# Performance work log

Measured on AMD Instinct MI355X. Metric: run time of the kernel, lower is better.

Reference implementation:

```python
import jax, jax.numpy as jnp
import numpy as np

EMBED_DIM = 256
NUM_HEADS = 4
HEAD_DIM = EMBED_DIM // NUM_HEADS
B, N0, N1 = 4, 2048, 2048


def setup_inputs() -> dict:
    key = jax.random.key(0)
    ks = jax.random.split(key, 16)
    d = EMBED_DIM
    s = 0.02
    return {
        "x0": jax.random.normal(ks[0], (B, N0, d), jnp.float32),
        "x1": jax.random.normal(ks[1], (B, N1, d), jnp.float32),
        "Wqk": jax.random.normal(ks[2], (d, d), jnp.float32) * s,
        "bqk": jnp.zeros((d,), jnp.float32),
        "Wv": jax.random.normal(ks[3], (d, d), jnp.float32) * s,
        "bv": jnp.zeros((d,), jnp.float32),
        "Wout": jax.random.normal(ks[4], (d, d), jnp.float32) * s,
        "bout": jnp.zeros((d,), jnp.float32),
        "W0": jax.random.normal(ks[5], (2 * d, 2 * d), jnp.float32) * s,
        "b0": jnp.zeros((2 * d,), jnp.float32),
        "ln_scale": jnp.ones((2 * d,), jnp.float32),
        "ln_bias": jnp.zeros((2 * d,), jnp.float32),
        "W3": jax.random.normal(ks[6], (2 * d, d), jnp.float32) * s,
        "b3": jnp.zeros((d,), jnp.float32),
    }


def _heads(t, b, n):
    # [b, n, d] -> [b, h, n, hd]
    return t.reshape(b, n, NUM_HEADS, HEAD_DIM).transpose(0, 2, 1, 3)


def _layernorm(y, scale, bias, eps=1e-5):
    mu = jnp.mean(y, axis=-1, keepdims=True)
    var = jnp.mean(jnp.square(y - mu), axis=-1, keepdims=True)
    return (y - mu) * jax.lax.rsqrt(var + eps) * scale + bias


def reference(x0, x1, Wqk, bqk, Wv, bv, Wout, bout, W0, b0, ln_scale, ln_bias, W3, b3):
    b, n0, d = x0.shape
    _, n1, _ = x1.shape
    scale = 1.0 / jnp.sqrt(jnp.float32(HEAD_DIM))

    qk0 = _heads(x0 @ Wqk + bqk, b, n0)
    qk1 = _heads(x1 @ Wqk + bqk, b, n1)
    v0 = _heads(x0 @ Wv + bv, b, n0)
    v1 = _heads(x1 @ Wv + bv, b, n1)

    # shared logits: [b, h, n0, n1]
    logits01 = jnp.einsum('bhid,bhjd->bhij', qk0, qk1) * scale
    attn01 = jax.nn.softmax(logits01, axis=-1)
    m0 = jnp.einsum('bhij,bhjd->bhid', attn01, v1)
    attn10 = jax.nn.softmax(logits01.transpose(0, 1, 3, 2), axis=-1)
    m1 = jnp.einsum('bhji,bhjd->bhid', attn10.transpose(0, 1, 3, 2), v0)

    m0 = m0.transpose(0, 2, 1, 3).reshape(b, n0, d) @ Wout + bout
    m1 = m1.transpose(0, 2, 1, 3).reshape(b, n1, d) @ Wout + bout

    def ffn(x, m):
        y = jnp.concatenate([x, m], axis=-1) @ W0 + b0
        y = _layernorm(y, ln_scale, ln_bias)
        y = jax.nn.gelu(y, approximate=False)
        return x + y @ W3 + b3

    return ffn(x0, m0), ffn(x1, m1)
```

## Files before the change

kernel.cpp:

```cpp
#include <hip/hip_runtime.h>
#include <math.h>

#define BATCH 4
#define SEQ 2048
#define DMODEL 256
#define NH 4
#define HD 64
#define MROWS 8192
#define QKSCALE 0.4246608905f

typedef short bf16x8 __attribute__((ext_vector_type(8)));
typedef float f32x4 __attribute__((ext_vector_type(4)));
typedef unsigned short us;

#if __has_builtin(__builtin_amdgcn_exp2f)
#define EXP2(x) __builtin_amdgcn_exp2f(x)
#else
#define EXP2(x) exp2f(x)
#endif

__device__ __forceinline__ us f2bf(float x) {
  union { float f; unsigned int u; } v;
  v.f = x;
  unsigned int r = (v.u + 0x7FFF + ((v.u >> 16) & 1)) >> 16;
  return (us)r;
}
__device__ __forceinline__ float bf2f(us u) {
  union { unsigned int u; float f; } v;
  v.u = ((unsigned int)u) << 16;
  return v.f;
}
__device__ __forceinline__ unsigned int fbits(float x) {
  union { float f; unsigned int u; } v;
  v.f = x;
  return v.u;
}
__device__ __forceinline__ unsigned int pk2bf(float lo, float hi) {
  return __builtin_amdgcn_perm(fbits(hi), fbits(lo), 0x07060302u);
}
__device__ __forceinline__ void dma16(const void* g, void* l) {
  auto gp = (const __attribute__((address_space(1))) unsigned int*)(unsigned long long)(uintptr_t)g;
  auto lp = (__attribute__((address_space(3))) unsigned int*)(unsigned int)(uintptr_t)l;
  __builtin_amdgcn_global_load_lds(gp, lp, 16, 0, 0);
}

__global__ __launch_bounds__(256) void cast_x(
    const float* __restrict__ x0, const float* __restrict__ x1,
    us* __restrict__ x0b, us* __restrict__ x1b) {
  const int n4 = (MROWS * DMODEL) / 4;
  int i = blockIdx.x * 256 + threadIdx.x;
  const float* src = (i < n4) ? x0 : x1;
  us* dst = (i < n4) ? x0b : x1b;
  int j = (i < n4) ? i : i - n4;
  float4 v = *(const float4*)&src[j * 4];
  ushort4 o = {f2bf(v.x), f2bf(v.y), f2bf(v.z), f2bf(v.w)};
  *(ushort4*)&dst[j * 4] = o;
}

__global__ __launch_bounds__(256) void cast_w(
    const float* __restrict__ Wqk, const float* __restrict__ Wv,
    const float* __restrict__ W0, const float* __restrict__ W3,
    const float* __restrict__ bqk, const float* __restrict__ bv,
    us* __restrict__ Wqvt, us* __restrict__ W1t, us* __restrict__ W3t,
    float* __restrict__ bias_qv) {
  int gid = blockIdx.x * 256 + threadIdx.x;
  if (gid < 65536) {
    int k = gid >> 8, j = gid & 255;
    Wqvt[j * 256 + k] = f2bf(Wqk[gid]);
  } else if (gid < 131072) {
    int i = gid - 65536;
    int k = i >> 8, j = i & 255;
    Wqvt[(256 + j) * 256 + k] = f2bf(Wv[i]);
  } else if (gid < 262144) {
    int i = gid - 131072;
    int k = i >> 9, j = i & 511;
    W1t[j * 512 + k] = f2bf(W0[i]);
  } else if (gid < 393216) {
    int i = gid - 262144;
    int k = i >> 8, j = i & 255;
    W3t[j * 512 + k] = f2bf(W3[i]);
  } else if (gid < 393728) {
    int j = gid - 393216;
    bias_qv[j] = (j < 256) ? bqk[j] : bv[j - 256];
  }
}

__global__ __launch_bounds__(256) void wcomb_k(
    const float* __restrict__ Wout, const float* __restrict__ W0,
    const float* __restrict__ b0, const float* __restrict__ bout,
    us* __restrict__ W1t, float* __restrict__ bias1) {
  int t = threadIdx.x, i = blockIdx.x;
  if (i < 256) {
    float a0 = 0.f, a1 = 0.f;
    for (int k0 = 0; k0 < 256; k0 += 8) {
      float wk[8], r0[8], r1[8];
#pragma unroll
      for (int u = 0; u < 8; ++u) {
        wk[u] = Wout[i * 256 + k0 + u];
        const float* row = &W0[(size_t)(256 + k0 + u) * 512];
        r0[u] = row[t];
        r1[u] = row[t + 256];
      }
#pragma unroll
      for (int u = 0; u < 8; ++u) { a0 += wk[u] * r0[u]; a1 += wk[u] * r1[u]; }
    }
    W1t[t * 512 + 256 + i] = f2bf(a0);
    W1t[(t + 256) * 512 + 256 + i] = f2bf(a1);
  } else {
    float a0 = b0[t], a1 = b0[t + 256];
    for (int k = 0; k < 256; ++k) {
      float bk = bout[k];
      const float* row = &W0[(size_t)(256 + k) * 512];
      a0 += bk * row[t];
      a1 += bk * row[t + 256];
    }
    bias1[t] = a0;
    bias1[t + 256] = a1;
  }
}

template <int MODE>
__global__ __launch_bounds__(256) void gemm4(
    const us* __restrict__ A0, const us* __restrict__ A1,
    const us* __restrict__ Am0, const us* __restrict__ Am1,
    const us* __restrict__ Wt, const float* __restrict__ bias,
    const float* __restrict__ r0_, const float* __restrict__ r1_,
    void* __restrict__ C0_, void* __restrict__ C1_,
    void* __restrict__ V0_, void* __restrict__ V1_, int K) {
  __shared__ us lds[17408];

  const int t = threadIdx.x, w = t >> 6, lane = t & 63;
  const int qd = lane >> 4, l15 = lane & 15;
  const int qr = w >> 1, qc = w & 1;
  const int row0 = blockIdx.x * 128;
  const int coltile = blockIdx.y, col0 = coltile * 128;
  const int z = blockIdx.z;
  const us* Ax = z ? A1 : A0;
  const us* Am = z ? Am1 : Am0;

  f32x4 acc[4][4];
#pragma unroll
  for (int i = 0; i < 4; ++i)
#pragma unroll
    for (int j = 0; j < 4; ++j) acc[i][j] = (f32x4){0.f, 0.f, 0.f, 0.f};

  for (int k0 = 0; k0 < K; k0 += 64) {
    __syncthreads();
#pragma unroll
    for (int pp = 0; pp < 8; ++pp) {
      int g = pp * 4 + w;
      const us* src;
      if (g < 16) {
        int tm = g >> 1, s = g & 1;
        const us* Ap = Ax;
        int kk = k0 + s * 32 + qd * 8;
        int lda = K;
        if (MODE == 1) {
          Ap = (k0 < 256) ? Ax : Am;
          kk = kk & 255;
          lda = 256;
        }
        src = &Ap[(size_t)(row0 + tm * 16 + l15) * lda + kk];
      } else {
        int gb = g - 16, tn = gb >> 1, s = gb & 1;
        src = &Wt[(size_t)(col0 + tn * 16 + l15) * K + k0 + s * 32 + qd * 8];
      }
      dma16(src, &lds[g * 512]);
    }
    __syncthreads();

#pragma unroll
    for (int s = 0; s < 2; ++s) {
      bf16x8 af[4], bfr[4];
#pragma unroll
      for (int i = 0; i < 4; ++i) {
        af[i] = *(const bf16x8*)&lds[(((qr * 4 + i) * 2 + s) * 64 + lane) * 8];
        bfr[i] = *(const bf16x8*)&lds[8192 + (((qc * 4 + i) * 2 + s) * 64 + lane) * 8];
      }
#pragma unroll
      for (int i = 0; i < 4; ++i)
#pragma unroll
        for (int j = 0; j < 4; ++j)
          acc[i][j] = __builtin_amdgcn_mfma_f32_16x16x32_bf16(af[i], bfr[j], acc[i][j], 0, 0, 0);
    }
  }

  if (MODE == 0 && coltile >= 2) {
    __syncthreads();
    int base = qc * 8320;
#pragma unroll
    for (int j = 0; j < 4; ++j) {
      int col = col0 + qc * 64 + j * 16 + l15;
      float bb = bias[col];
#pragma unroll
      for (int i = 0; i < 4; ++i)
#pragma unroll
        for (int r = 0; r < 4; ++r)
          lds[base + (j * 16 + l15) * 130 + (qr * 64 + i * 16 + qd * 4 + r)] =
              f2bf(acc[i][j][r] + bb);
    }
    __syncthreads();
    us* Vt = (us*)(z ? V1_ : V0_);
    int b_ = row0 >> 11, seq0 = row0 & 2047;
    for (int c = t; c < 2048; c += 256) {
      int hh = c >> 10, cc = c & 1023;
      int dloc = cc >> 4, scc = cc & 15;
      int h = (coltile - 2) * 2 + hh;
      uint4 d = *(const uint4*)&lds[hh * 8320 + dloc * 130 + scc * 8];
      *(uint4*)&Vt[((size_t)(b_ * NH + h) * HD + dloc) * SEQ + seq0 + scc * 8] = d;
    }
    return;
  }

#pragma unroll
  for (int j = 0; j < 4; ++j) {
    int col = col0 + qc * 64 + j * 16 + l15;
    float bb = bias[col];
#pragma unroll
    for (int i = 0; i < 4; ++i)
#pragma unroll
      for (int r = 0; r < 4; ++r) {
        size_t grow = row0 + qr * 64 + i * 16 + qd * 4 + r;
        float v = acc[i][j][r] + bb;
        if (MODE == 0) {
          ((us*)(z ? C1_ : C0_))[grow * 256 + col] = f2bf(v * QKSCALE);
        } else if (MODE == 1) {
          ((us*)(z ? C1_ : C0_))[grow * 512 + col] = f2bf(v);
        } else {
          const float* R = z ? r1_ : r0_;
          ((float*)(z ? C1_ : C0_))[grow * 256 + col] = R[grow * 256 + col] + v;
        }
      }
  }
}

__global__ __launch_bounds__(256) void flash_v6(
    const us* __restrict__ qk0, const us* __restrict__ qk1,
    const us* __restrict__ vt0, const us* __restrict__ vt1,
    float* __restrict__ Opart, float* __restrict__ lpart) {
  __shared__ us lds[16384];
  const int t = threadIdx.x, w = t >> 6, lane = t & 63;
  const int qd = lane >> 4, l15 = lane & 15;
  const int qt = blockIdx.x & 15, half = blockIdx.x >> 4;
  const int h = blockIdx.y, z = blockIdx.z, dir = z & 1, b = z >> 1;
  const us* Qb = dir ? qk1 : qk0;
  const us* Kb = dir ? qk0 : qk1;
  const us* Vt = dir ? vt0 : vt1;
  float* Op = Opart + (size_t)(dir * 2 + half) * (MROWS * DMODEL);
  float* lp = lpart + ((size_t)(dir * 2 + half) * NH + h) * MROWS;
  const size_t qrow0 = (size_t)b * SEQ + (size_t)qt * 128;
  const int hoff = h * HD;
  const us* vtb = Vt + (size_t)(b * NH + h) * HD * SEQ;
  const int kt0 = half * 16;

  const us* sp[4];
  int sstr[4];
#pragma unroll
  for (int pp = 0; pp < 4; ++pp) {
    int g = pp * 4 + w;
    if (g < 8) {
      int tk = g >> 1, s = g & 1;
      int kvl = (tk >> 1) * 32 + (l15 >> 2) * 8 + (tk & 1) * 4 + (l15 & 3);
      sp[pp] = &Kb[(size_t)(b * SEQ + kt0 * 64 + kvl) * DMODEL + hoff + s * 32 + qd * 8];
      sstr[pp] = 64 * DMODEL;
    } else {
      int td = (g - 8) >> 1, s = g & 1;
      sp[pp] = &vtb[(size_t)(td * 16 + l15) * SEQ + kt0 * 64 + s * 32 + qd * 8];
      sstr[pp] = 64;
    }
  }

  bf16x8 qf[2][2];
#pragma unroll
  for (int qh = 0; qh < 2; ++qh)
#pragma unroll
    for (int s = 0; s < 2; ++s)
      qf[qh][s] = *(const bf16x8*)&Qb[(qrow0 + w * 32 + qh * 16 + l15) * DMODEL + hoff + s * 32 + qd * 8];

  f32x4 Oacc[2][4];
#pragma unroll
  for (int qh = 0; qh < 2; ++qh)
#pragma unroll
    for (int td = 0; td < 4; ++td) Oacc[qh][td] = (f32x4){0.f, 0.f, 0.f, 0.f};
  float l_lane[2] = {0.f, 0.f};

#pragma unroll
  for (int pp = 0; pp < 4; ++pp) {
    dma16(sp[pp], &lds[(pp * 4 + w) * 512]);
    sp[pp] += sstr[pp];
  }
  __syncthreads();

  int bsel = 0;
  for (int it = 0; it < 16; ++it) {
    if (it < 15) {
#pragma unroll
      for (int pp = 0; pp < 4; ++pp) {
        dma16(sp[pp], &lds[(bsel ^ 1) * 8192 + (pp * 4 + w) * 512]);
        sp[pp] += sstr[pp];
      }
    }
    const us* L = &lds[bsel * 8192];

    bf16x8 kf[4][2], vf[4][2];
#pragma unroll
    for (int tk = 0; tk < 4; ++tk)
#pragma unroll
      for (int s = 0; s < 2; ++s) {
        kf[tk][s] = *(const bf16x8*)&L[((tk * 2 + s) * 64 + lane) * 8];
        vf[tk][s] = *(const bf16x8*)&L[((8 + tk * 2 + s) * 64 + lane) * 8];
      }

#pragma unroll
    for (int qh = 0; qh < 2; ++qh) {
      f32x4 S[4];
#pragma unroll
      for (int tk = 0; tk < 4; ++tk) {
        f32x4 a = {0.f, 0.f, 0.f, 0.f};
        a = __builtin_amdgcn_mfma_f32_16x16x32_bf16(kf[tk][0], qf[qh][0], a, 0, 0, 0);
        a = __builtin_amdgcn_mfma_f32_16x16x32_bf16(kf[tk][1], qf[qh][1], a, 0, 0, 0);
        S[tk] = a;
      }
      float p[4][4];
      float rs = 0.f;
#pragma unroll
      for (int tk = 0; tk < 4; ++tk)
#pragma unroll
        for (int r = 0; r < 4; ++r) {
          float pv = EXP2(S[tk][r]);
          p[tk][r] = pv;
          rs += pv;
        }
      l_lane[qh] += rs;
      union { bf16x8 v; unsigned int u[4]; } pk0, pk1;
      pk0.u[0] = pk2bf(p[0][0], p[0][1]);
      pk0.u[1] = pk2bf(p[0][2], p[0][3]);
      pk0.u[2] = pk2bf(p[1][0], p[1][1]);
      pk0.u[3] = pk2bf(p[1][2], p[1][3]);
      pk1.u[0] = pk2bf(p[2][0], p[2][1]);
      pk1.u[1] = pk2bf(p[2][2], p[2][3]);
      pk1.u[2] = pk2bf(p[3][0], p[3][1]);
      pk1.u[3] = pk2bf(p[3][2], p[3][3]);
#pragma unroll
      for (int td = 0; td < 4; ++td) {
        Oacc[qh][td] = __builtin_amdgcn_mfma_f32_16x16x32_bf16(pk0.v, vf[td][0], Oacc[qh][td], 0, 0, 0);
        Oacc[qh][td] = __builtin_amdgcn_mfma_f32_16x16x32_bf16(pk1.v, vf[td][1], Oacc[qh][td], 0, 0, 0);
      }
    }
    __syncthreads();
    bsel ^= 1;
  }

#pragma unroll
  for (int qh = 0; qh < 2; ++qh) {
    float l = l_lane[qh];
    l += __shfl_xor(l, 16);
    l += __shfl_xor(l, 32);
    if (qd == 0) lp[qrow0 + w * 32 + qh * 16 + l15] = l;
#pragma unroll
    for (int r = 0; r < 4; ++r) {
      size_t row = qrow0 + w * 32 + qh * 16 + qd * 4 + r;
#pragma unroll
      for (int td = 0; td < 4; ++td)
        Op[row * DMODEL + hoff + td * 16 + l15] = Oacc[qh][td][r];
    }
  }
}

__global__ __launch_bounds__(256) void combine_k(
    const float* __restrict__ Opart, const float* __restrict__ lpart,
    us* __restrict__ m0b, us* __restrict__ m1b) {
  int gid = blockIdx.x * 256 + threadIdx.x;
  int dir = gid >= (MROWS * DMODEL / 4);
  int idx = gid - dir * (MROWS * DMODEL / 4);
  int row = idx >> 6;
  int c4 = (idx & 63) << 2;
  int h = c4 >> 6;
  const float* Oa = Opart + (size_t)(dir * 2 + 0) * (MROWS * DMODEL);
  const float* Ob = Opart + (size_t)(dir * 2 + 1) * (MROWS * DMODEL);
  float la = lpart[((size_t)(dir * 2 + 0) * NH + h) * MROWS + row];
  float lb = lpart[((size_t)(dir * 2 + 1) * NH + h) * MROWS + row];
  float inv = 1.0f / (la + lb);
  float4 a = *(const float4*)&Oa[(size_t)row * DMODEL + c4];
  float4 bv = *(const float4*)&Ob[(size_t)row * DMODEL + c4];
  us* m = dir ? m1b : m0b;
  ushort4 o = {f2bf((a.x + bv.x) * inv), f2bf((a.y + bv.y) * inv),
               f2bf((a.z + bv.z) * inv), f2bf((a.w + bv.w) * inv)};
  *(ushort4*)&m[(size_t)row * DMODEL + c4] = o;
}

__global__ __launch_bounds__(256) void ln_gelu3(
    us* __restrict__ Y0, us* __restrict__ Y1,
    const float* __restrict__ sc, const float* __restrict__ bi) {
  int w = threadIdx.x >> 6, lane = threadIdx.x & 63;
  int ridx = blockIdx.x * 4 + w;
  us* Y = (ridx >= MROWS) ? Y1 : Y0;
  int row = ridx & (MROWS - 1);
  us* p = Y + (size_t)row * 512 + lane * 8;
  uint4 u = *(const uint4*)p;
  unsigned int uu[4] = {u.x, u.y, u.z, u.w};
  float v[8];
#pragma unroll
  for (int i = 0; i < 4; ++i) {
    v[2 * i] = bf2f((us)(uu[i] & 0xFFFF));
    v[2 * i + 1] = bf2f((us)(uu[i] >> 16));
  }
  float s1 = 0.f, s2 = 0.f;
#pragma unroll
  for (int i = 0; i < 8; ++i) { s1 += v[i]; s2 += v[i] * v[i]; }
#pragma unroll
  for (int m = 1; m < 64; m <<= 1) {
    s1 += __shfl_xor(s1, m);
    s2 += __shfl_xor(s2, m);
  }
  float mu = s1 * (1.0f / 512.0f);
  float var = s2 * (1.0f / 512.0f) - mu * mu;
  float rstd = rsqrtf(var + 1e-5f);
  int c0 = lane * 8;
  float4 scA = *(const float4*)&sc[c0], scB = *(const float4*)&sc[c0 + 4];
  float4 biA = *(const float4*)&bi[c0], biB = *(const float4*)&bi[c0 + 4];
  float scv[8] = {scA.x, scA.y, scA.z, scA.w, scB.x, scB.y, scB.z, scB.w};
  float biv[8] = {biA.x, biA.y, biA.z, biA.w, biB.x, biB.y, biB.z, biB.w};
  unsigned int ou[4];
#pragma unroll
  for (int i = 0; i < 4; ++i) {
    float y0 = (v[2 * i] - mu) * rstd * scv[2 * i] + biv[2 * i];
    float y1 = (v[2 * i + 1] - mu) * rstd * scv[2 * i + 1] + biv[2 * i + 1];
    y0 = 0.5f * y0 * (1.0f + erff(y0 * 0.70710678118654752f));
    y1 = 0.5f * y1 * (1.0f + erff(y1 * 0.70710678118654752f));
    ou[i] = (unsigned int)f2bf(y0) | ((unsigned int)f2bf(y1) << 16);
  }
  uint4 o = {ou[0], ou[1], ou[2], ou[3]};
  *(uint4*)p = o;
}

extern "C" void kernel_launch(void* const* d_in, const int* in_sizes, int n_in,
                              void* d_out, int out_size, void* d_ws,
                              size_t ws_size, hipStream_t stream) {
  const float* x0   = (const float*)d_in[0];
  const float* x1   = (const float*)d_in[1];
  const float* Wqk  = (const float*)d_in[2];
  const float* bqk  = (const float*)d_in[3];
  const float* Wv   = (const float*)d_in[4];
  const float* bv   = (const float*)d_in[5];
  const float* Wout = (const float*)d_in[6];
  const float* bout = (const float*)d_in[7];
  const float* W0   = (const float*)d_in[8];
  const float* b0   = (const float*)d_in[9];
  const float* lns  = (const float*)d_in[10];
  const float* lnb  = (const float*)d_in[11];
  const float* W3   = (const float*)d_in[12];
  const float* b3   = (const float*)d_in[13];

  char* ws = (char*)d_ws;
  const size_t MB = 1024 * 1024;
  us* x0b  = (us*)(ws + 0 * MB);
  us* x1b  = (us*)(ws + 4 * MB);
  us* Wqvt = (us*)(ws + 8 * MB);
  us* W1t  = (us*)(ws + 8 * MB + 262144);
  us* W3t  = (us*)(ws + 8 * MB + 786432);
  float* bias_qv = (float*)(ws + 9 * MB);
  float* bias1   = (float*)(ws + 9 * MB + 4096);
  us* qk0b = (us*)(ws + 10 * MB);
  us* qk1b = (us*)(ws + 14 * MB);
  us* vt0  = (us*)(ws + 18 * MB);
  us* vt1  = (us*)(ws + 22 * MB);
  us* m0b  = (us*)(ws + 26 * MB);
  us* m1b  = (us*)(ws + 30 * MB);
  us* y0b  = (us*)(ws + 10 * MB);
  us* y1b  = (us*)(ws + 18 * MB);
  float* Opart = (float*)(ws + 34 * MB);
  float* lpart = (float*)(ws + 66 * MB);
  float* out0 = (float*)d_out;
  float* out1 = out0 + (size_t)MROWS * DMODEL;

  dim3 blk(256);

  cast_x<<<dim3(4096), blk, 0, stream>>>(x0, x1, x0b, x1b);
  cast_w<<<dim3(1538), blk, 0, stream>>>(Wqk, Wv, W0, W3, bqk, bv,
                                         Wqvt, W1t, W3t, bias_qv);
  wcomb_k<<<dim3(257), blk, 0, stream>>>(Wout, W0, b0, bout, W1t, bias1);

  gemm4<0><<<dim3(64, 4, 2), blk, 0, stream>>>(
      x0b, x1b, nullptr, nullptr, Wqvt, bias_qv, nullptr, nullptr,
      qk0b, qk1b, vt0, vt1, 256);

  flash_v6<<<dim3(32, 4, 8), blk, 0, stream>>>(qk0b, qk1b, vt0, vt1, Opart, lpart);
  combine_k<<<dim3(4096), blk, 0, stream>>>(Opart, lpart, m0b, m1b);

  gemm4<1><<<dim3(64, 4, 2), blk, 0, stream>>>(
      x0b, x1b, m0b, m1b, W1t, bias1, nullptr, nullptr,
      y0b, y1b, nullptr, nullptr, 512);

  ln_gelu3<<<dim3(4096), blk, 0, stream>>>(y0b, y1b, lns, lnb);

  gemm4<2><<<dim3(64, 2, 2), blk, 0, stream>>>(
      y0b, y1b, nullptr, nullptr, W3t, b3, x0, x1,
      out0, out1, nullptr, nullptr, 512);
}
```

Measured before the change: 229.1 us.

## Fuse prep kernels, double-buffer GEMM loads, remap blocks to XCDs, split final GEMM

Merges the three preprocessing kernels (input cast, weight cast/transpose, Wout·W0 combination) into one launch to cut launch overhead. The GEMM now double-buffers its LDS tiles so the next K-slice's global-to-LDS DMA overlaps the current MFMA work. Both the GEMM and the flash-attention kernel remap the flat block index so that blocks sharing data land on the same XCD, aiming at better L2 reuse. The final GEMM uses 64-wide column tiles to double its block count. Costs are twice the LDS footprint, which may lower occupancy, and a prologue that hardcodes the first-tile pointer.

Measured after the change: 233.3 us. Within noise of the previous version (+1.9%).

```diff
diff --git a/kernel.cpp b/kernel.cpp
--- a/kernel.cpp
+++ b/kernel.cpp
@@ -44,149 +44,176 @@
   __builtin_amdgcn_global_load_lds(gp, lp, 16, 0, 0);
 }
 
-__global__ __launch_bounds__(256) void cast_x(
+__global__ __launch_bounds__(256) void prep_k(
     const float* __restrict__ x0, const float* __restrict__ x1,
-    us* __restrict__ x0b, us* __restrict__ x1b) {
-  const int n4 = (MROWS * DMODEL) / 4;
-  int i = blockIdx.x * 256 + threadIdx.x;
-  const float* src = (i < n4) ? x0 : x1;
-  us* dst = (i < n4) ? x0b : x1b;
-  int j = (i < n4) ? i : i - n4;
-  float4 v = *(const float4*)&src[j * 4];
-  ushort4 o = {f2bf(v.x), f2bf(v.y), f2bf(v.z), f2bf(v.w)};
-  *(ushort4*)&dst[j * 4] = o;
-}
-
-__global__ __launch_bounds__(256) void cast_w(
     const float* __restrict__ Wqk, const float* __restrict__ Wv,
     const float* __restrict__ W0, const float* __restrict__ W3,
+    const float* __restrict__ Wout,
     const float* __restrict__ bqk, const float* __restrict__ bv,
+    const float* __restrict__ b0, const float* __restrict__ bout,
+    us* __restrict__ x0b, us* __restrict__ x1b,
     us* __restrict__ Wqvt, us* __restrict__ W1t, us* __restrict__ W3t,
-    float* __restrict__ bias_qv) {
-  int gid = blockIdx.x * 256 + threadIdx.x;
-  if (gid < 65536) {
-    int k = gid >> 8, j = gid & 255;
-    Wqvt[j * 256 + k] = f2bf(Wqk[gid]);
-  } else if (gid < 131072) {
-    int i = gid - 65536;
-    int k = i >> 8, j = i & 255;
-    Wqvt[(256 + j) * 256 + k] = f2bf(Wv[i]);
-  } else if (gid < 262144) {
-    int i = gid - 131072;
-    int k = i >> 9, j = i & 511;
-    W1t[j * 512 + k] = f2bf(W0[i]);
-  } else if (gid < 393216) {
-    int i = gid - 262144;
-    int k = i >> 8, j = i & 255;
-    W3t[j * 512 + k] = f2bf(W3[i]);
-  } else if (gid < 393728) {
-    int j = gid - 393216;
-    bias_qv[j] = (j < 256) ? bqk[j] : bv[j - 256];
-  }
-}
-
-__global__ __launch_bounds__(256) void wcomb_k(
-    const float* __restrict__ Wout, const float* __restrict__ W0,
-    const float* __restrict__ b0, const float* __restrict__ bout,
-    us* __restrict__ W1t, float* __restrict__ bias1) {
-  int t = threadIdx.x, i = blockIdx.x;
-  if (i < 256) {
-    float a0 = 0.f, a1 = 0.f;
-    for (int k0 = 0; k0 < 256; k0 += 8) {
-      float wk[8], r0[8], r1[8];
-#pragma unroll
-      for (int u = 0; u < 8; ++u) {
-        wk[u] = Wout[i * 256 + k0 + u];
-        const float* row = &W0[(size_t)(256 + k0 + u) * 512];
-        r0[u] = row[t];
-        r1[u] = row[t + 256];
-      }
-#pragma unroll
-      for (int u = 0; u < 8; ++u) { a0 += wk[u] * r0[u]; a1 += wk[u] * r1[u]; }
-    }
-    W1t[t * 512 + 256 + i] = f2bf(a0);
-    W1t[(t + 256) * 512 + 256 + i] = f2bf(a1);
+    float* __restrict__ bias_qv, float* __restrict__ bias1) {
+  const int bid = blockIdx.x, t = threadIdx.x;
+  if (bid < 4096) {
+    const int n4 = (MROWS * DMODEL) / 4;
+    int i = bid * 256 + t;
+    const float* src = (i < n4) ? x0 : x1;
+    us* dst = (i < n4) ? x0b : x1b;
+    int j = (i < n4) ? i : i - n4;
+    float4 v = *(const float4*)&src[j * 4];
+    ushort4 o = {f2bf(v.x), f2bf(v.y), f2bf(v.z), f2bf(v.w)};
+    *(ushort4*)&dst[j * 4] = o;
+  } else if (bid < 5634) {
+    int gid = (bid - 4096) * 256 + t;
+    if (gid < 65536) {
+      int k = gid >> 8, j = gid & 255;
+      Wqvt[j * 256 + k] = f2bf(Wqk[gid]);
+    } else if (gid < 131072) {
+      int i = gid - 65536;
+      int k = i >> 8, j = i & 255;
+      Wqvt[(256 + j) * 256 + k] = f2bf(Wv[i]);
+    } else if (gid < 262144) {
+      int i = gid - 131072;
+      int k = i >> 9, j = i & 511;
+      W1t[j * 512 + k] = f2bf(W0[i]);
+    } else if (gid < 393216) {
+      int i = gid - 262144;
+      int k = i >> 8, j = i & 255;
+      W3t[j * 512 + k] = f2bf(W3[i]);
+    } else if (gid < 393728) {
+      int j = gid - 393216;
+      bias_qv[j] = (j < 256) ? bqk[j] : bv[j - 256];
+    }
   } else {
-    float a0 = b0[t], a1 = b0[t + 256];
-    for (int k = 0; k < 256; ++k) {
-      float bk = bout[k];
-      const float* row = &W0[(size_t)(256 + k) * 512];
-      a0 += bk * row[t];
-      a1 += bk * row[t + 256];
-    }
-    bias1[t] = a0;
-    bias1[t + 256] = a1;
+    int i = bid - 5634;
+    if (i < 256) {
+      float a0 = 0.f, a1 = 0.f;
+      for (int k0 = 0; k0 < 256; k0 += 8) {
+        float wk[8], r0[8], r1[8];
+#pragma unroll
+        for (int u = 0; u < 8; ++u) {
+          wk[u] = Wout[i * 256 + k0 + u];
+          const float* row = &W0[(size_t)(256 + k0 + u) * 512];
+          r0[u] = row[t];
+          r1[u] = row[t + 256];
+        }
+#pragma unroll
+        for (int u = 0; u < 8; ++u) { a0 += wk[u] * r0[u]; a1 += wk[u] * r1[u]; }
+      }
+      W1t[t * 512 + 256 + i] = f2bf(a0);
+      W1t[(t + 256) * 512 + 256 + i] = f2bf(a1);
+    } else {
+      float a0 = b0[t], a1 = b0[t + 256];
+      for (int k = 0; k < 256; ++k) {
+        float bk = bout[k];
+        const float* row = &W0[(size_t)(256 + k) * 512];
+        a0 += bk * row[t];
+        a1 += bk * row[t + 256];
+      }
+      bias1[t] = a0;
+      bias1[t + 256] = a1;
+    }
   }
 }
 
 template <int MODE>
-__global__ __launch_bounds__(256) void gemm4(
+__global__ __launch_bounds__(256) void gemm5(
     const us* __restrict__ A0, const us* __restrict__ A1,
     const us* __restrict__ Am0, const us* __restrict__ Am1,
     const us* __restrict__ Wt, const float* __restrict__ bias,
     const float* __restrict__ r0_, const float* __restrict__ r1_,
     void* __restrict__ C0_, void* __restrict__ C1_,
     void* __restrict__ V0_, void* __restrict__ V1_, int K) {
-  __shared__ us lds[17408];
+  constexpr int CT = (MODE == 2) ? 64 : 128;
+  constexpr int BG = (CT / 16) * 2;
+  constexpr int BUFS = 8192 + BG * 512;
+  __shared__ us lds[2 * BUFS];
 
   const int t = threadIdx.x, w = t >> 6, lane = t & 63;
   const int qd = lane >> 4, l15 = lane & 15;
-  const int qr = w >> 1, qc = w & 1;
-  const int row0 = blockIdx.x * 128;
-  const int coltile = blockIdx.y, col0 = coltile * 128;
-  const int z = blockIdx.z;
+
+  const int flat = blockIdx.x + 64 * (blockIdx.y + 4 * blockIdx.z);
+  const int xcd = flat & 7, slot = flat >> 3;
+  const int xz = (xcd << 4) + (slot >> 2);
+  const int bx = xz & 63, z = xz >> 6, coltile = slot & 3;
+  const int row0 = bx * 128, col0 = coltile * CT;
+
   const us* Ax = z ? A1 : A0;
   const us* Am = z ? Am1 : Am0;
-
-  f32x4 acc[4][4];
-#pragma unroll
-  for (int i = 0; i < 4; ++i)
+  const int qr = (MODE == 2) ? w : (w >> 1);
+  const int qc = (MODE == 2) ? 0 : (w & 1);
+  constexpr int MI = (MODE == 2) ? 2 : 4;
+
+  f32x4 acc[MI][4];
+#pragma unroll
+  for (int i = 0; i < MI; ++i)
 #pragma unroll
     for (int j = 0; j < 4; ++j) acc[i][j] = (f32x4){0.f, 0.f, 0.f, 0.f};
 
-  for (int k0 = 0; k0 < K; k0 += 64) {
-    __syncthreads();
-#pragma unroll
-    for (int pp = 0; pp < 8; ++pp) {
-      int g = pp * 4 + w;
-      const us* src;
-      if (g < 16) {
-        int tm = g >> 1, s = g & 1;
-        const us* Ap = Ax;
-        int kk = k0 + s * 32 + qd * 8;
-        int lda = K;
-        if (MODE == 1) {
-          Ap = (k0 < 256) ? Ax : Am;
-          kk = kk & 255;
-          lda = 256;
+  const int NK = K >> 6;
+#pragma unroll
+  for (int pp = 0; pp < (16 + BG) / 4; ++pp) {
+    int g = pp * 4 + w;
+    const us* src;
+    if (g < 16) {
+      int tm = g >> 1, s = g & 1;
+      int kk = s * 32 + qd * 8;
+      src = &((MODE == 1) ? Ax : Ax)[(size_t)(row0 + tm * 16 + l15) * ((MODE == 1) ? 256 : K) + kk];
+    } else {
+      int gb = g - 16, tn = gb >> 1, s = gb & 1;
+      src = &Wt[(size_t)(col0 + tn * 16 + l15) * K + s * 32 + qd * 8];
+    }
+    dma16(src, &lds[g * 512]);
+  }
+  __syncthreads();
+
+  int bsel = 0;
+  for (int it = 0; it < NK; ++it) {
+    if (it + 1 < NK) {
+      int k0 = (it + 1) << 6;
+#pragma unroll
+      for (int pp = 0; pp < (16 + BG) / 4; ++pp) {
+        int g = pp * 4 + w;
+        const us* src;
+        if (g < 16) {
+          int tm = g >> 1, s = g & 1;
+          const us* Ap = Ax;
+          int kk = k0 + s * 32 + qd * 8, lda = K;
+          if (MODE == 1) {
+            Ap = (k0 < 256) ? Ax : Am;
+            kk &= 255;
+            lda = 256;
+          }
+          src = &Ap[(size_t)(row0 + tm * 16 + l15) * lda + kk];
+        } else {
+          int gb = g - 16, tn = gb >> 1, s = gb & 1;
+          src = &Wt[(size_t)(col0 + tn * 16 + l15) * K + k0 + s * 32 + qd * 8];
         }
-        src = &Ap[(size_t)(row0 + tm * 16 + l15) * lda + kk];
-      } else {
-        int gb = g - 16, tn = gb >> 1, s = gb & 1;
-        src = &Wt[(size_t)(col0 + tn * 16 + l15) * K + k0 + s * 32 + qd * 8];
-      }
-      dma16(src, &lds[g * 512]);
-    }
-    __syncthreads();
-
+        dma16(src, &lds[(bsel ^ 1) * BUFS + g * 512]);
+      }
+    }
+    const us* L = &lds[bsel * BUFS];
 #pragma unroll
     for (int s = 0; s < 2; ++s) {
-      bf16x8 af[4], bfr[4];
-#pragma unroll
-      for (int i = 0; i < 4; ++i) {
-        af[i] = *(const bf16x8*)&lds[(((qr * 4 + i) * 2 + s) * 64 + lane) * 8];
-        bfr[i] = *(const bf16x8*)&lds[8192 + (((qc * 4 + i) * 2 + s) * 64 + lane) * 8];
-      }
-#pragma unroll
-      for (int i = 0; i < 4; ++i)
+      bf16x8 af[MI], bfr[4];
+#pragma unroll
+      for (int i = 0; i < MI; ++i)
+        af[i] = *(const bf16x8*)&L[(((qr * MI + i) * 2 + s) * 64 + lane) * 8];
+#pragma unroll
+      for (int j = 0; j < 4; ++j)
+        bfr[j] = *(const bf16x8*)&L[8192 + (((qc * 4 + j) * 2 + s) * 64 + lane) * 8];
+#pragma unroll
+      for (int i = 0; i < MI; ++i)
 #pragma unroll
         for (int j = 0; j < 4; ++j)
           acc[i][j] = __builtin_amdgcn_mfma_f32_16x16x32_bf16(af[i], bfr[j], acc[i][j], 0, 0, 0);
     }
+    __syncthreads();
+    bsel ^= 1;
   }
 
   if (MODE == 0 && coltile >= 2) {
-    __syncthreads();
     int base = qc * 8320;
 #pragma unroll
     for (int j = 0; j < 4; ++j) {
@@ -217,10 +244,10 @@
     int col = col0 + qc * 64 + j * 16 + l15;
     float bb = bias[col];
 #pragma unroll
-    for (int i = 0; i < 4; ++i)
+    for (int i = 0; i < MI; ++i)
 #pragma unroll
       for (int r = 0; r < 4; ++r) {
-        size_t grow = row0 + qr * 64 + i * 16 + qd * 4 + r;
+        size_t grow = row0 + qr * (MI * 16) + i * 16 + qd * 4 + r;
         float v = acc[i][j][r] + bb;
         if (MODE == 0) {
           ((us*)(z ? C1_ : C0_))[grow * 256 + col] = f2bf(v * QKSCALE);
@@ -234,15 +261,21 @@
   }
 }
 
-__global__ __launch_bounds__(256) void flash_v6(
+__global__ __launch_bounds__(256) void flash_v7(
     const us* __restrict__ qk0, const us* __restrict__ qk1,
     const us* __restrict__ vt0, const us* __restrict__ vt1,
     float* __restrict__ Opart, float* __restrict__ lpart) {
   __shared__ us lds[16384];
   const int t = threadIdx.x, w = t >> 6, lane = t & 63;
   const int qd = lane >> 4, l15 = lane & 15;
-  const int qt = blockIdx.x & 15, half = blockIdx.x >> 4;
-  const int h = blockIdx.y, z = blockIdx.z, dir = z & 1, b = z >> 1;
+
+  const int flat = blockIdx.x + 32 * (blockIdx.y + 4 * blockIdx.z);
+  const int xcd = flat & 7, slot = flat >> 3;
+  const int combo = (xcd << 2) + (slot >> 5);
+  const int qs = slot & 31;
+  const int qt = qs & 15, half = qs >> 4;
+  const int dir = combo >> 4, bh = combo & 15, b = bh >> 2, h = bh & 3;
+
   const us* Qb = dir ? qk1 : qk0;
   const us* Kb = dir ? qk0 : qk1;
   const us* Vt = dir ? vt0 : vt1;
@@ -476,25 +509,25 @@
 
   dim3 blk(256);
 
-  cast_x<<<dim3(4096), blk, 0, stream>>>(x0, x1, x0b, x1b);
-  cast_w<<<dim3(1538), blk, 0, stream>>>(Wqk, Wv, W0, W3, bqk, bv,
-                                         Wqvt, W1t, W3t, bias_qv);
-  wcomb_k<<<dim3(257), blk, 0, stream>>>(Wout, W0, b0, bout, W1t, bias1);
-
-  gemm4<0><<<dim3(64, 4, 2), blk, 0, stream>>>(
+  prep_k<<<dim3(5891), blk, 0, stream>>>(x0, x1, Wqk, Wv, W0, W3, Wout,
+                                         bqk, bv, b0, bout,
+                                         x0b, x1b, Wqvt, W1t, W3t,
+                                         bias_qv, bias1);
+
+  gemm5<0><<<dim3(64, 4, 2), blk, 0, stream>>>(
       x0b, x1b, nullptr, nullptr, Wqvt, bias_qv, nullptr, nullptr,
       qk0b, qk1b, vt0, vt1, 256);
 
-  flash_v6<<<dim3(32, 4, 8), blk, 0, stream>>>(qk0b, qk1b, vt0, vt1, Opart, lpart);
+  flash_v7<<<dim3(32, 4, 8), blk, 0, stream>>>(qk0b, qk1b, vt0, vt1, Opart, lpart);
   combine_k<<<dim3(4096), blk, 0, stream>>>(Opart, lpart, m0b, m1b);
 
-  gemm4<1><<<dim3(64, 4, 2), blk, 0, stream>>>(
+  gemm5<1><<<dim3(64, 4, 2), blk, 0, stream>>>(
       x0b, x1b, m0b, m1b, W1t, bias1, nullptr, nullptr,
       y0b, y1b, nullptr, nullptr, 512);
 
   ln_gelu3<<<dim3(4096), blk, 0, stream>>>(y0b, y1b, lns, lnb);
 
-  gemm4<2><<<dim3(64, 2, 2), blk, 0, stream>>>(
+  gemm5<2><<<dim3(64, 4, 2), blk, 0, stream>>>(
       y0b, y1b, nullptr, nullptr, W3t, b3, x0, x1,
       out0, out1, nullptr, nullptr, 512);
 }
```
